# Optimization experiments

Hardware: AMD Instinct MI355X
Metric: run time of the kernel (lower is better)

The kernel has to match this reference:

```python
import jax, jax.numpy as jnp
import numpy as np

NV, NG, D, K, NB = 4096, 2048, 64, 128, 4
C_IN, C_OUT, E = 128, 8, 32768
SIGMA = 2.5  # rbf sigma used in the non-mp path


def _gcn_conv(x, src, dst, w, b, n):
    # PyG GCNConv (edge_weight=None, self loops already appended to src/dst)
    deg = jax.ops.segment_sum(jnp.ones(src.shape, x.dtype), dst, num_segments=n)
    dinv = jnp.where(deg > 0, 1.0 / jnp.sqrt(deg), 0.0)
    norm = dinv[src] * dinv[dst]
    h = x @ w
    return jax.ops.segment_sum(h[src] * norm[:, None], dst, num_segments=n) + b


def _diff_block(x, mass, evals, evecs, gradX, gradY, t, a_re, a_im, w0, b0, w1, b1, w2, b2):
    # learned-time spectral diffusion
    x_spec = evecs.T @ (x * mass[:, None])                      # [K, D]
    coef = jnp.exp(-evals[:, None] * jnp.clip(t, 1e-8)[None, :])  # [K, D]
    x_diff = evecs @ (coef * x_spec)                            # [NV, D]
    # spatial gradient features: complex grad, learned rotation, tanh of inner product
    gX = gradX @ x_diff                                         # real part  [NV, D]
    gY = gradY @ x_diff                                         # imag part  [NV, D]
    b_re = gX @ a_re - gY @ a_im
    b_im = gY @ a_re + gX @ a_im
    gfeat = jnp.tanh(gX * b_re + gY * b_im)
    f = jnp.concatenate([x, x_diff, gfeat], axis=-1)            # [NV, 3D]
    h = jax.nn.relu(f @ w0 + b0)
    h = jax.nn.relu(h @ w1 + b1)
    return h @ w2 + b2 + x                                      # residual skip


def _forward(surf_x, mass, evals, evecs, gradX, gradY, vertices, graph_x, graph_pos,
             lin1_w, lin1_b, lin2_w, lin2_b, last_w, last_b,
             diff_time, A_re, A_im, mlp_w0, mlp_b0, mlp_w1, mlp_b1, mlp_w2, mlp_b2,
             gcn_w1, gcn_b1, gcn_w2, gcn_b2, edge_index):
    nv, ng = vertices.shape[0], graph_pos.shape[0]
    # dense rbf coupling (torch.no_grad in original -> stop_gradient)
    d2 = (jnp.sum(vertices * vertices, 1)[:, None]
          + jnp.sum(graph_pos * graph_pos, 1)[None, :]
          - 2.0 * (vertices @ graph_pos.T))
    dist = jnp.sqrt(jnp.clip(d2, 0.0))
    rbf = jax.lax.stop_gradient(jnp.exp(-dist / SIGMA))          # [NV, NG]
    diff_x = surf_x @ lin1_w + lin1_b                            # [NV, D]
    gx = graph_x @ lin2_w + lin2_b                               # [NG, D]
    loops = jnp.arange(ng, dtype=edge_index.dtype)
    src = jnp.concatenate([edge_index[0], loops])
    dst = jnp.concatenate([edge_index[1], loops])
    for i in range(NB):
        diff_x = _diff_block(diff_x, mass, evals, evecs, gradX, gradY,
                             diff_time[i], A_re[i], A_im[i],
                             mlp_w0[i], mlp_b0[i], mlp_w1[i], mlp_b1[i], mlp_w2[i], mlp_b2[i])
        gx = rbf.T @ diff_x                                      # surface -> graph
        h = jax.nn.relu(_gcn_conv(gx, src, dst, gcn_w1[i], gcn_b1[i], ng))
        gx = _gcn_conv(h, src, dst, gcn_w2[i], gcn_b2[i], ng)
        diff_x = rbf @ gx                                        # graph -> surface
    return diff_x @ last_w + last_b                              # [NV, C_OUT]


def setup_inputs() -> dict:
    key = jax.random.key(0)
    ks = jax.random.split(key, 24)
    f32 = jnp.float32
    def rn(k, shape, scale=1.0):
        return jax.random.normal(k, shape, f32) * scale
    inp = {
        'surf_x': rn(ks[0], (NV, 5)),
        'mass': jax.random.uniform(ks[1], (NV,), f32, 0.1, 1.0),
        'evals': jnp.sort(jax.random.uniform(ks[2], (K,), f32, 0.0, 50.0)),
        'evecs': rn(ks[3], (NV, K), 1.0 / np.sqrt(NV)),
        'gradX': rn(ks[4], (NV, NV), 1.0 / np.sqrt(NV)),
        'gradY': rn(ks[5], (NV, NV), 1.0 / np.sqrt(NV)),
        'vertices': rn(ks[6], (NV, 3), 5.0),
        'graph_x': rn(ks[7], (NG, C_IN)),
        'graph_pos': rn(ks[8], (NG, 3), 5.0),
        'lin1_w': rn(ks[9], (5, D), 1.0 / np.sqrt(5)),
        'lin1_b': jnp.zeros((D,), f32),
        'lin2_w': rn(ks[10], (C_IN, D), 1.0 / np.sqrt(C_IN)),
        'lin2_b': jnp.zeros((D,), f32),
        'last_w': rn(ks[11], (D, C_OUT), 1.0 / np.sqrt(D)),
        'last_b': jnp.zeros((C_OUT,), f32),
        'diff_time': jax.random.uniform(ks[12], (NB, D), f32, 1e-3, 1.0),
        'A_re': rn(ks[13], (NB, D, D), 1.0 / np.sqrt(D)),
        'A_im': rn(ks[14], (NB, D, D), 1.0 / np.sqrt(D)),
        'mlp_w0': rn(ks[15], (NB, 3 * D, D), 1.0 / np.sqrt(3 * D)),
        'mlp_b0': jnp.zeros((NB, D), f32),
        'mlp_w1': rn(ks[16], (NB, D, D), 1.0 / np.sqrt(D)),
        'mlp_b1': jnp.zeros((NB, D), f32),
        'mlp_w2': rn(ks[17], (NB, D, D), 1.0 / np.sqrt(D)),
        'mlp_b2': jnp.zeros((NB, D), f32),
        'gcn_w1': rn(ks[18], (NB, D, D), 1.0 / np.sqrt(D)),
        'gcn_b1': jnp.zeros((NB, D), f32),
        'gcn_w2': rn(ks[19], (NB, D, D), 1.0 / np.sqrt(D)),
        'gcn_b2': jnp.zeros((NB, D), f32),
        'edge_index': jax.random.randint(ks[20], (2, E), 0, NG, dtype=jnp.int32),
    }
    return inp


def reference(surf_x, mass, evals, evecs, gradX, gradY, vertices, graph_x, graph_pos,
              lin1_w, lin1_b, lin2_w, lin2_b, last_w, last_b,
              diff_time, A_re, A_im, mlp_w0, mlp_b0, mlp_w1, mlp_b1, mlp_w2, mlp_b2,
              gcn_w1, gcn_b1, gcn_w2, gcn_b2, edge_index):
    return _forward(surf_x, mass, evals, evecs, gradX, gradY, vertices, graph_x, graph_pos,
                    lin1_w, lin1_b, lin2_w, lin2_b, last_w, last_b,
                    diff_time, A_re, A_im, mlp_w0, mlp_b0, mlp_w1, mlp_b1, mlp_w2, mlp_b2,
                    gcn_w1, gcn_b1, gcn_w2, gcn_b2, edge_index)
```

## Files before the change

### kernel.cpp

```cpp
#include <hip/hip_runtime.h>
#include <hip/hip_bf16.h>

#define NVV 4096
#define NGG 2048
#define DD 64
#define KSP 128
#define NBLK 4
#define NEDGE 32768
#define COUT 8
#define NSLICE 8
#define NSLICE_G 16
#define NSLICE_V 8
#define NSLICE_S 32
#define VS 32

typedef __hip_bfloat16 bf16;
using bf16x8 = __attribute__((ext_vector_type(8))) __bf16;
using s16x8  = __attribute__((ext_vector_type(8))) short;
using f32x4  = __attribute__((ext_vector_type(4))) float;

__device__ __forceinline__ float toF(bf16 x){ return __bfloat162float(x); }
__device__ __forceinline__ float ldin(const void* p, size_t i, int f){
  return f ? toF(((const bf16*)p)[i]) : ((const float*)p)[i];
}
__device__ __forceinline__ short f2bf(float x){
  __bf16 b = (__bf16)x;
  return __builtin_bit_cast(short, b);
}
__device__ __forceinline__ float bf2f(short s){
  return (float)__builtin_bit_cast(__bf16, s);
}
__device__ __forceinline__ bf16x8 ld8(const short* p){
  return __builtin_bit_cast(bf16x8, *(const s16x8*)p);
}
__device__ __forceinline__ void gl16(const short* g, short* l){
  __builtin_amdgcn_global_load_lds((__attribute__((address_space(1))) void*)(g),
                                   (__attribute__((address_space(3))) void*)(l),
                                   16, 0, 0);
}

__global__ void k_probe(const void* __restrict__ mass, int* __restrict__ flag){
  int t = threadIdx.x;
  float v = toF(((const bf16*)mass)[t]);
  bool ok = (v >= 0.05f) && (v <= 1.05f);
  unsigned long long m = __ballot(ok);
  if (t == 0) flag[0] = (m == ~0ull) ? 1 : 0;
}

__global__ void k_csr_zero(int* c){ int g = blockIdx.x*256+threadIdx.x; if (g<NGG) c[g]=0; }
__global__ void k_csr_cnt(const int* __restrict__ ei, int* __restrict__ c){
  int e = blockIdx.x*256+threadIdx.x; if (e<NEDGE) atomicAdd(&c[ei[NEDGE+e]], 1);
}
__global__ void k_csr_scan(const int* __restrict__ cnt, int* __restrict__ off,
                           int* __restrict__ cursor, float* __restrict__ dinv){
  __shared__ int ws[256];
  int t = threadIdx.x;
  int base = t*8;
  int local[8]; int s = 0;
  #pragma unroll
  for (int i=0;i<8;i++){ local[i]=s; s += cnt[base+i]; }
  ws[t] = s;
  __syncthreads();
  for (int o=1;o<256;o<<=1){
    int v = (t>=o) ? ws[t-o] : 0;
    __syncthreads();
    ws[t] += v;
    __syncthreads();
  }
  int pre = (t==0) ? 0 : ws[t-1];
  #pragma unroll
  for (int i=0;i<8;i++){
    int o = pre + local[i];
    off[base+i] = o; cursor[base+i] = o;
    dinv[base+i] = rsqrtf(1.f + (float)cnt[base+i]);
  }
  if (t==255) off[NGG] = pre + s;
}
__global__ void k_csr_fill(const int* __restrict__ ei, int* __restrict__ cursor,
                           int* __restrict__ csrc){
  int e = blockIdx.x*256+threadIdx.x;
  if (e < NEDGE){
    int d = ei[NEDGE+e];
    int p = atomicAdd(&cursor[d], 1);
    csrc[p] = ei[e];
  }
}

__global__ void k_lin1_mx(const void* __restrict__ sx, const void* __restrict__ w,
                          const void* __restrict__ b, const void* __restrict__ mass,
                          float* __restrict__ out, short* __restrict__ btMX,
                          const int* __restrict__ flg){
  const int f = *flg;
  __shared__ short tl[64*68];
  const int t = threadIdx.x;
  const int r = t>>2, c0 = (t&3)*16;
  const size_t v = (size_t)blockIdx.x*64 + r;
  float sxa[5];
  #pragma unroll
  for (int k=0;k<5;k++) sxa[k] = ldin(sx, v*5+k, f);
  const float mv = ldin(mass, v, f);
  float acc[16];
  #pragma unroll
  for (int j=0;j<16;j++){
    float a = ldin(b, c0+j, f);
    #pragma unroll
    for (int k=0;k<5;k++) a += sxa[k]*ldin(w, (size_t)k*DD + c0 + j, f);
    acc[j] = a;
    tl[(size_t)(c0+j)*68 + r] = f2bf(a*mv);
  }
  float* op = out + v*DD + c0;
  ((float4*)op)[0] = *(float4*)&acc[0];
  ((float4*)op)[1] = *(float4*)&acc[4];
  ((float4*)op)[2] = *(float4*)&acc[8];
  ((float4*)op)[3] = *(float4*)&acc[12];
  __syncthreads();
  s16x8 u0, u1;
  #pragma unroll
  for (int j=0;j<8;j++){ u0[j]=tl[(size_t)r*68+c0+j]; u1[j]=tl[(size_t)r*68+c0+8+j]; }
  const int s8 = (r&7)<<3;
  short* dp = btMX + (size_t)blockIdx.x*4096 + (size_t)r*64;
  *(s16x8*)&dp[c0 ^ s8]     = u0;
  *(s16x8*)&dp[(c0+8) ^ s8] = u1;
}

__global__ void k_spec_red(const float* __restrict__ partial, const void* __restrict__ evals,
                           const void* __restrict__ tvec, int boff,
                           short* __restrict__ btA, const int* __restrict__ flg){
  const int f = *flg;
  int idx = blockIdx.x*256 + threadIdx.x;
  int k = idx >> 6, d = idx & 63;
  float sum = 0.f;
  #pragma unroll 8
  for (int s = 0; s < VS; s++) sum += partial[(size_t)s*KSP*DD + idx];
  float t = fmaxf(ldin(tvec, boff + d, f), 1e-8f);
  float val = expf(-ldin(evals, k, f) * t) * sum;
  btA[(size_t)(k>>6)*4096 + (size_t)d*64 + ((k&63) ^ ((d&7)<<3))] = f2bf(val);
}

__global__ void k_cvt_a(const void* __restrict__ src, short* __restrict__ dst,
                        int Kfull, const int* __restrict__ flg){
  const int f = *flg;
  const int t = threadIdx.x;
  const int r = t>>2, c0 = (t&3)*16;
  const size_t row = (size_t)blockIdx.x*64 + r;
  const size_t base = row*(size_t)Kfull + (size_t)blockIdx.y*64 + c0;
  s16x8 v0, v1;
  if (f){
    const short* sp = (const short*)src + base;
    v0 = ((const s16x8*)sp)[0];
    v1 = ((const s16x8*)sp)[1];
  } else {
    const float* sp = (const float*)src + base;
    float tmp[16];
    ((float4*)tmp)[0] = ((const float4*)sp)[0];
    ((float4*)tmp)[1] = ((const float4*)sp)[1];
    ((float4*)tmp)[2] = ((const float4*)sp)[2];
    ((float4*)tmp)[3] = ((const float4*)sp)[3];
    #pragma unroll
    for (int i=0;i<8;i++){ v0[i]=f2bf(tmp[i]); v1[i]=f2bf(tmp[8+i]); }
  }
  const int s8 = (r&7)<<3;
  short* dp = dst + ((size_t)blockIdx.x*(Kfull>>6) + blockIdx.y)*4096 + (size_t)r*64;
  *(s16x8*)&dp[c0 ^ s8]     = v0;
  *(s16x8*)&dp[(c0+8) ^ s8] = v1;
}

__global__ void k_cvt_at(const void* __restrict__ evecs, short* __restrict__ dst,
                         const int* __restrict__ flg){
  const int f = *flg;
  __shared__ short tl[64*68];
  const int t = threadIdx.x;
  const int r = t>>2, c0 = (t&3)*16;
  const int kt = blockIdx.x, s = blockIdx.y;
  const size_t v = (size_t)kt*64 + r;
  #pragma unroll
  for (int j=0;j<16;j++)
    tl[(size_t)(c0+j)*68 + r] = f2bf(ldin(evecs, v*KSP + (size_t)s*64 + c0 + j, f));
  __syncthreads();
  s16x8 u0, u1;
  #pragma unroll
  for (int j=0;j<8;j++){ u0[j]=tl[(size_t)r*68+c0+j]; u1[j]=tl[(size_t)r*68+c0+8+j]; }
  const int s8 = (r&7)<<3;
  short* dp = dst + ((size_t)s*64 + kt)*4096 + (size_t)r*64;
  *(s16x8*)&dp[c0 ^ s8]     = u0;
  *(s16x8*)&dp[(c0+8) ^ s8] = u1;
}

__global__ void k_rbf_pre(const void* __restrict__ P, const void* __restrict__ Q,
                          short* __restrict__ rbfV, short* __restrict__ rbfG,
                          const int* __restrict__ flg){
  const int f = *flg;
  __shared__ short tl[64*68];
  const int t = threadIdx.x;
  const int r = t>>2, c0 = (t&3)*16;
  const int vt = blockIdx.x, gt = blockIdx.y;
  const float px = ldin(P, ((size_t)vt*64+r)*3+0, f);
  const float py = ldin(P, ((size_t)vt*64+r)*3+1, f);
  const float pz = ldin(P, ((size_t)vt*64+r)*3+2, f);
  s16x8 v0, v1;
  #pragma unroll
  for (int j=0;j<16;j++){
    const size_t g = (size_t)gt*64 + c0 + j;
    float dx = px - ldin(Q, g*3+0, f);
    float dy = py - ldin(Q, g*3+1, f);
    float dz = pz - ldin(Q, g*3+2, f);
    short s = f2bf(__expf(-sqrtf(dx*dx+dy*dy+dz*dz)*0.4f));
    if (j<8) v0[j] = s; else v1[j-8] = s;
    tl[(size_t)(c0+j)*68 + r] = s;
  }
  const int s8 = (r&7)<<3;
  short* vp = rbfV + ((size_t)vt*(NGG/64) + gt)*4096 + (size_t)r*64;
  *(s16x8*)&vp[c0 ^ s8]     = v0;
  *(s16x8*)&vp[(c0+8) ^ s8] = v1;
  __syncthreads();
  s16x8 u0, u1;
  #pragma unroll
  for (int j=0;j<8;j++){ u0[j] = tl[(size_t)r*68 + c0 + j]; u1[j] = tl[(size_t)r*68 + c0 + 8 + j]; }
  short* gp = rbfG + ((size_t)gt*(NVV/64) + vt)*4096 + (size_t)r*64;
  *(s16x8*)&gp[c0 ^ s8]     = u0;
  *(s16x8*)&gp[(c0+8) ^ s8] = u1;
}

__global__ void k_cvt_wt(const void* __restrict__ Are, const void* __restrict__ Aim,
                         const void* __restrict__ w0, const void* __restrict__ w1,
                         const void* __restrict__ w2,
                         short* __restrict__ btRe, short* __restrict__ btIm,
                         short* __restrict__ btW0, short* __restrict__ btW1,
                         short* __restrict__ btW2, const int* __restrict__ flg){
  const int f = *flg;
  __shared__ short tl[64*68];
  const int t = threadIdx.x;
  const int r = t>>2, c0 = (t&3)*16;
  const int slot = blockIdx.x, b = blockIdx.y;
  const void* src; size_t soff; short* dst; float scale = 1.f;
  switch(slot){
    case 0: src=Are; soff=(size_t)b*4096; dst=btRe + (size_t)b*2*4096;               break;
    case 1: src=Aim; soff=(size_t)b*4096; dst=btRe + (size_t)b*2*4096 + 4096; scale=-1.f; break;
    case 2: src=Aim; soff=(size_t)b*4096; dst=btIm + (size_t)b*2*4096;               break;
    case 3: src=Are; soff=(size_t)b*4096; dst=btIm + (size_t)b*2*4096 + 4096;        break;
    case 4: case 5: case 6:
      src=w0; soff=(size_t)b*3*4096 + (size_t)(slot-4)*4096;
      dst=btW0 + (size_t)b*3*4096 + (size_t)(slot-4)*4096;                           break;
    case 7: src=w1; soff=(size_t)b*4096; dst=btW1 + (size_t)b*4096;                  break;
    default: src=w2; soff=(size_t)b*4096; dst=btW2 + (size_t)b*4096;                 break;
  }
  #pragma unroll
  for (int j=0;j<16;j++)
    tl[(size_t)(c0+j)*68 + r] = f2bf(scale * ldin(src, soff + (size_t)r*64 + c0 + j, f));
  __syncthreads();
  s16x8 u0, u1;
  #pragma unroll
  for (int j=0;j<8;j++){ u0[j]=tl[(size_t)r*68+c0+j]; u1[j]=tl[(size_t)r*68+c0+8+j]; }
  const int s8 = (r&7)<<3;
  short* dp = dst + (size_t)r*64;
  *(s16x8*)&dp[c0 ^ s8]     = u0;
  *(s16x8*)&dp[(c0+8) ^ s8] = u1;
}

template<int TWO>
__global__ void k_gemm_pre(const short* __restrict__ A0, const short* __restrict__ A1,
                           const short* __restrict__ Bt, float* __restrict__ C,
                           int M, int ktt, int tps, int yoff, short* __restrict__ btOut){
  constexpr int NBUF = TWO ? 3 : 2;
  __shared__ __align__(16) short sm[2*NBUF*4096];
  const int t = threadIdx.x;
  const int w = t>>6, lane = t&63;
  const int fr = lane&15, fq = lane>>4;
  const int strip = blockIdx.x, sl = blockIdx.y;
  const size_t abase = ((size_t)strip*ktt + (size_t)sl*tps)*4096;
  const short* gA0 = A0 + abase;
  const short* gA1 = TWO ? (A1 + abase) : A0;
  const short* gB  = Bt + (size_t)sl*tps*4096;
  const int to = t*8;

  auto stage = [&](int p, int kt){
    short* l = &sm[p*NBUF*4096];
    const size_t ko = (size_t)kt*4096;
    gl16(gA0 + ko + to,        l + (w<<9));
    gl16(gA0 + ko + 2048 + to, l + 2048 + (w<<9));
    if (TWO){
      gl16(gA1 + ko + to,        l + 4096 + (w<<9));
      gl16(gA1 + ko + 2048 + to, l + 6144 + (w<<9));
    }
    short* lb = l + (TWO ? 8192 : 4096);
    gl16(gB + ko + to,        lb + (w<<9));
    gl16(gB + ko + 2048 + to, lb + 2048 + (w<<9));
  };

  f32x4 acc0[4] = {{0,0,0,0},{0,0,0,0},{0,0,0,0},{0,0,0,0}};
  f32x4 acc1[4] = {{0,0,0,0},{0,0,0,0},{0,0,0,0},{0,0,0,0}};

  stage(0, 0);
  int cur = 0;
  const int arow = w*16 + fr;
  const int ax0 = arow*64;
  const int asw = (arow&7)<<3;
  for (int kt=0; kt<tps; ++kt){
    if (kt+1 < tps){
      stage(cur^1, kt+1);
      if constexpr (TWO) asm volatile("s_waitcnt vmcnt(6)" ::: "memory");
      else               asm volatile("s_waitcnt vmcnt(4)" ::: "memory");
    } else {
      asm volatile("s_waitcnt vmcnt(0)" ::: "memory");
    }
    __builtin_amdgcn_s_barrier();
    asm volatile("" ::: "memory");
    const short* As  = &sm[cur*NBUF*4096];
    const short* A1s = As + 4096;
    const short* Bs  = As + (TWO ? 8192 : 4096);
    #pragma unroll
    for (int ks=0; ks<2; ks++){
      const int kx = ks*32 + fq*8;
      bf16x8 a0 = ld8(&As[ax0 + (kx ^ asw)]);
      bf16x8 a1 = TWO ? ld8(&A1s[ax0 + (kx ^ asw)]) : a0;
      #pragma unroll
      for (int nc=0;nc<4;nc++){
        const int brow = nc*16 + fr;
        bf16x8 b = ld8(&Bs[brow*64 + (kx ^ ((brow&7)<<3))]);
        acc0[nc] = __builtin_amdgcn_mfma_f32_16x16x32_bf16(a0, b, acc0[nc], 0, 0, 0);
        if constexpr (TWO)
          acc1[nc] = __builtin_amdgcn_mfma_f32_16x16x32_bf16(a1, b, acc1[nc], 0, 0, 0);
      }
    }
    asm volatile("" ::: "memory");
    __builtin_amdgcn_s_barrier();
    cur ^= 1;
  }
  float* C0 = C + (size_t)sl*M*DD;
  const int row0 = strip*64 + w*16 + fq*4;
  #pragma unroll
  for (int nc=0;nc<4;nc++)
    #pragma unroll
    for (int r=0;r<4;r++)
      C0[(size_t)(row0+r)*DD + nc*16 + fr] = acc0[nc][r];
  if constexpr (TWO){
    float* C1 = C + (size_t)yoff + (size_t)sl*M*DD;
    #pragma unroll
    for (int nc=0;nc<4;nc++)
      #pragma unroll
      for (int r=0;r<4;r++)
        C1[(size_t)(row0+r)*DD + nc*16 + fr] = acc1[nc][r];
  }
  if (btOut){
    #pragma unroll
    for (int nc=0;nc<4;nc++)
      #pragma unroll
      for (int r=0;r<4;r++){
        int k = row0 + r, n = nc*16 + fr;
        btOut[(size_t)(k>>6)*4096 + (size_t)n*64 + ((k&63) ^ ((n&7)<<3))] = f2bf(acc0[nc][r]);
      }
  }
}

__global__ void k_reduce_mx(const float* __restrict__ P, const void* __restrict__ mass,
                            float* __restrict__ C, short* __restrict__ btMX,
                            int slices, const int* __restrict__ flg){
  const int f = *flg;
  __shared__ short tl[64*68];
  const int t = threadIdx.x;
  const int r = t>>2, c0 = (t&3)*16;
  const size_t v = (size_t)blockIdx.x*64 + r;
  float acc[16];
  #pragma unroll
  for (int j=0;j<16;j++) acc[j] = 0.f;
  const float* pb = P + v*DD + c0;
  for (int s=0;s<slices;s++){
    const float* ps = pb + (size_t)s*NVV*DD;
    #pragma unroll
    for (int q=0;q<4;q++){
      float4 a = ((const float4*)ps)[q];
      acc[q*4+0]+=a.x; acc[q*4+1]+=a.y; acc[q*4+2]+=a.z; acc[q*4+3]+=a.w;
    }
  }
  float* op = C + v*DD + c0;
  ((float4*)op)[0] = *(float4*)&acc[0];
  ((float4*)op)[1] = *(float4*)&acc[4];
  ((float4*)op)[2] = *(float4*)&acc[8];
  ((float4*)op)[3] = *(float4*)&acc[12];
  const float mv = ldin(mass, v, f);
  #pragma unroll
  for (int j=0;j<16;j++) tl[(size_t)(c0+j)*68 + r] = f2bf(acc[j]*mv);
  __syncthreads();
  s16x8 u0, u1;
  #pragma unroll
  for (int j=0;j<8;j++){ u0[j]=tl[(size_t)r*68+c0+j]; u1[j]=tl[(size_t)r*68+c0+8+j]; }
  const int s8 = (r&7)<<3;
  short* dp = btMX + (size_t)blockIdx.x*4096 + (size_t)r*64;
  *(s16x8*)&dp[c0 ^ s8]     = u0;
  *(s16x8*)&dp[(c0+8) ^ s8] = u1;
}

__global__ void k_tail_fused(const float* __restrict__ part,
                             const float* __restrict__ cur, const float* __restrict__ xdiff,
                             const short* __restrict__ btRe, const short* __restrict__ btIm,
                             const short* __restrict__ btW0, const short* __restrict__ btW1,
                             const short* __restrict__ btW2,
                             const void* __restrict__ b0, const void* __restrict__ b1,
                             const void* __restrict__ b2, int boff,
                             short* __restrict__ btOut, const int* __restrict__ flg){
  __shared__ __align__(16) short sm[8*4096];
  const int f = *flg;
  const int t = threadIdx.x;
  const int w = t>>6, lane = t&63;
  const int fr = lane&15, fq = lane>>4;
  const int strip = blockIdx.x;
  const int to = t*8;
  gl16(btRe + to,        &sm[2*4096] + (w<<9));
  gl16(btRe + 2048 + to, &sm[2*4096] + 2048 + (w<<9));
  gl16(btRe + 4096 + to, &sm[3*4096] + (w<<9));
  gl16(btRe + 6144 + to, &sm[3*4096] + 2048 + (w<<9));
  gl16(btIm + to,        &sm[4*4096] + (w<<9));
  gl16(btIm + 2048 + to, &sm[4*4096] + 2048 + (w<<9));
  gl16(btIm + 4096 + to, &sm[5*4096] + (w<<9));
  gl16(btIm + 6144 + to, &sm[5*4096] + 2048 + (w<<9));
  {
    const int r = t>>2, c0 = (t&3)*16;
    float4 gxa[4] = {{0,0,0,0},{0,0,0,0},{0,0,0,0},{0,0,0,0}};
    float4 gya[4] = {{0,0,0,0},{0,0,0,0},{0,0,0,0},{0,0,0,0}};
    const float* pb = part + ((size_t)strip*64 + r)*DD + c0;
    #pragma unroll
    for (int s=0;s<NSLICE;s++){
      const float* px = pb + (size_t)s*NVV*DD;
      const float* py = pb + (size_t)(s+NSLICE)*NVV*DD;
      #pragma unroll
      for (int q=0;q<4;q++){
        float4 a = ((const float4*)px)[q];
        float4 bq = ((const float4*)py)[q];
        gxa[q].x+=a.x;  gxa[q].y+=a.y;  gxa[q].z+=a.z;  gxa[q].w+=a.w;
        gya[q].x+=bq.x; gya[q].y+=bq.y; gya[q].z+=bq.z; gya[q].w+=bq.w;
      }
    }
    const float* gx_ = (const float*)gxa;
    const float* gy_ = (const float*)gya;
    s16x8 x0,x1,y0,y1;
    #pragma unroll
    for (int j=0;j<8;j++){ x0[j]=f2bf(gx_[j]); x1[j]=f2bf(gx_[8+j]);
                           y0[j]=f2bf(gy_[j]); y1[j]=f2bf(gy_[8+j]); }
    const int s8 = (r&7)<<3;
    *(s16x8*)&sm[0*4096 + r*64 + (c0 ^ s8)]     = x0;
    *(s16x8*)&sm[0*4096 + r*64 + ((c0+8) ^ s8)] = x1;
    *(s16x8*)&sm[1*4096 + r*64 + (c0 ^ s8)]     = y0;
    *(s16x8*)&sm[1*4096 + r*64 + ((c0+8) ^ s8)] = y1;
    const float* cp = cur   + ((size_t)strip*64 + r)*DD + c0;
    const float* xp = xdiff + ((size_t)strip*64 + r)*DD + c0;
    float ca[16], xa[16];
    ((float4*)ca)[0]=((const float4*)cp)[0]; ((float4*)ca)[1]=((const float4*)cp)[1];
    ((float4*)ca)[2]=((const float4*)cp)[2]; ((float4*)ca)[3]=((const float4*)cp)[3];
    ((float4*)xa)[0]=((const float4*)xp)[0]; ((float4*)xa)[1]=((const float4*)xp)[1];
    ((float4*)xa)[2]=((const float4*)xp)[2]; ((float4*)xa)[3]=((const float4*)xp)[3];
    s16x8 v0,v1,u0,u1;
    #pragma unroll
    for (int j=0;j<8;j++){ v0[j]=f2bf(ca[j]); v1[j]=f2bf(ca[8+j]);
                           u0[j]=f2bf(xa[j]); u1[j]=f2bf(xa[8+j]); }
    *(s16x8*)&sm[6*4096 + r*64 + (c0 ^ s8)]     = v0;
    *(s16x8*)&sm[6*4096 + r*64 + ((c0+8) ^ s8)] = v1;
    *(s16x8*)&sm[7*4096 + r*64 + (c0 ^ s8)]     = u0;
    *(s16x8*)&sm[7*4096 + r*64 + ((c0+8) ^ s8)] = u1;
  }
  __syncthreads();
  const int arow = w*16 + fr;
  const int asw = (arow&7)<<3;
  f32x4 re[4] = {{0,0,0,0},{0,0,0,0},{0,0,0,0},{0,0,0,0}};
  f32x4 im[4] = {{0,0,0,0},{0,0,0,0},{0,0,0,0},{0,0,0,0}};
  #pragma unroll
  for (int kt=0; kt<2; kt++){
    const short* As = &sm[kt*4096];
    const short* Br = &sm[(2+kt)*4096];
    const short* Bi = &sm[(4+kt)*4096];
    #pragma unroll
    for (int ks=0; ks<2; ks++){
      const int kx = ks*32 + fq*8;
      bf16x8 a = ld8(&As[arow*64 + (kx ^ asw)]);
      #pragma unroll
      for (int nc=0;nc<4;nc++){
        const int brow = nc*16 + fr, bsw = (brow&7)<<3;
        bf16x8 br_ = ld8(&Br[brow*64 + (kx ^ bsw)]);
        bf16x8 bi_ = ld8(&Bi[brow*64 + (kx ^ bsw)]);
        re[nc] = __builtin_amdgcn_mfma_f32_16x16x32_bf16(a, br_, re[nc], 0, 0, 0);
        im[nc] = __builtin_amdgcn_mfma_f32_16x16x32_bf16(a, bi_, im[nc], 0, 0, 0);
      }
    }
  }
  __syncthreads();
  gl16(btW0 + to,           &sm[2*4096] + (w<<9));
  gl16(btW0 + 2048 + to,    &sm[2*4096] + 2048 + (w<<9));
  gl16(btW0 + 4096 + to,    &sm[3*4096] + (w<<9));
  gl16(btW0 + 6144 + to,    &sm[3*4096] + 2048 + (w<<9));
  gl16(btW0 + 8192 + to,    &sm[4*4096] + (w<<9));
  gl16(btW0 + 10240 + to,   &sm[4*4096] + 2048 + (w<<9));
  gl16(btW1 + to,           &sm[5*4096] + (w<<9));
  gl16(btW1 + 2048 + to,    &sm[5*4096] + 2048 + (w<<9));
  float gfv[4][4];
  #pragma unroll
  for (int nc=0;nc<4;nc++){
    const int n = nc*16 + fr;
    #pragma unroll
    for (int r2=0;r2<4;r2++){
      const int mi = w*16 + fq*4 + r2;
      const int pos = mi*64 + (n ^ ((mi&7)<<3));
      float gx = bf2f(sm[pos]);
      float gy = bf2f(sm[4096 + pos]);
      gfv[nc][r2] = tanhf(gx*re[nc][r2] + gy*im[nc][r2]);
    }
  }
  __syncthreads();
  gl16(btW2 + to,        &sm[1*4096] + (w<<9));
  gl16(btW2 + 2048 + to, &sm[1*4096] + 2048 + (w<<9));
  #pragma unroll
  for (int nc=0;nc<4;nc++)
    #pragma unroll
    for (int r2=0;r2<4;r2++){
      const int mi = w*16 + fq*4 + r2, n = nc*16 + fr;
      sm[mi*64 + (n ^ ((mi&7)<<3))] = f2bf(gfv[nc][r2]);
    }
  __syncthreads();
  f32x4 acc[4] = {{0,0,0,0},{0,0,0,0},{0,0,0,0},{0,0,0,0}};
  #pragma unroll
  for (int kt=0; kt<3; kt++){
    const short* As = &sm[(kt==0 ? 6 : (kt==1 ? 7 : 0))*4096];
    const short* Bs = &sm[(2+kt)*4096];
    #pragma unroll
    for (int ks=0; ks<2; ks++){
      const int kx = ks*32 + fq*8;
      bf16x8 a = ld8(&As[arow*64 + (kx ^ asw)]);
      #pragma unroll
      for (int nc=0;nc<4;nc++){
        const int brow = nc*16 + fr;
        bf16x8 b = ld8(&Bs[brow*64 + (kx ^ ((brow&7)<<3))]);
        acc[nc] = __builtin_amdgcn_mfma_f32_16x16x32_bf16(a, b, acc[nc], 0, 0, 0);
      }
    }
  }
  __syncthreads();
  #pragma unroll
  for (int nc=0;nc<4;nc++){
    float bz = ldin(b0, boff + nc*16 + fr, f);
    #pragma unroll
    for (int r2=0;r2<4;r2++){
      const int mi = w*16 + fq*4 + r2, n = nc*16 + fr;
      sm[6*4096 + mi*64 + (n ^ ((mi&7)<<3))] = f2bf(fmaxf(acc[nc][r2] + bz, 0.f));
    }
  }
  __syncthreads();
  f32x4 a1c[4] = {{0,0,0,0},{0,0,0,0},{0,0,0,0},{0,0,0,0}};
  #pragma unroll
  for (int ks=0; ks<2; ks++){
    const int kx = ks*32 + fq*8;
    bf16x8 a = ld8(&sm[6*4096 + arow*64 + (kx ^ asw)]);
    #pragma unroll
    for (int nc=0;nc<4;nc++){
      const int brow = nc*16 + fr;
      bf16x8 b = ld8(&sm[5*4096 + brow*64 + (kx ^ ((brow&7)<<3))]);
      a1c[nc] = __builtin_amdgcn_mfma_f32_16x16x32_bf16(a, b, a1c[nc], 0, 0, 0);
    }
  }
  #pragma unroll
  for (int nc=0;nc<4;nc++){
    float bz = ldin(b1, boff + nc*16 + fr, f);
    #pragma unroll
    for (int r2=0;r2<4;r2++){
      const int mi = w*16 + fq*4 + r2, n = nc*16 + fr;
      sm[7*4096 + mi*64 + (n ^ ((mi&7)<<3))] = f2bf(fmaxf(a1c[nc][r2] + bz, 0.f));
    }
  }
  __syncthreads();
  f32x4 a2c[4] = {{0,0,0,0},{0,0,0,0},{0,0,0,0},{0,0,0,0}};
  #pragma unroll
  for (int ks=0; ks<2; ks++){
    const int kx = ks*32 + fq*8;
    bf16x8 a = ld8(&sm[7*4096 + arow*64 + (kx ^ asw)]);
    #pragma unroll
    for (int nc=0;nc<4;nc++){
      const int brow = nc*16 + fr;
      bf16x8 b = ld8(&sm[1*4096 + brow*64 + (kx ^ ((brow&7)<<3))]);
      a2c[nc] = __builtin_amdgcn_mfma_f32_16x16x32_bf16(a, b, a2c[nc], 0, 0, 0);
    }
  }
  const int row0 = strip*64 + w*16 + fq*4;
  #pragma unroll
  for (int nc=0;nc<4;nc++){
    float bz = ldin(b2, boff + nc*16 + fr, f);
    #pragma unroll
    for (int r2=0;r2<4;r2++){
      int row = row0 + r2, n = nc*16 + fr;
      float vv = a2c[nc][r2] + bz + cur[(size_t)row*DD + n];
      btOut[(size_t)(row>>6)*4096 + (size_t)n*64 + ((row&63) ^ ((n&7)<<3))] = f2bf(vv);
    }
  }
}

__global__ void k_gcn1(const float* __restrict__ part, const void* __restrict__ W,
                       int woff, const float* __restrict__ dinv,
                       const void* __restrict__ bias, int boff,
                       float* __restrict__ tmp, float* __restrict__ outinit,
                       const int* __restrict__ flg){
  const int f = *flg;
  __shared__ float xs[4][DD];
  int d = threadIdx.x & 63, vl = threadIdx.x >> 6;
  size_t g = (size_t)blockIdx.x*4 + vl;
  float x = 0.f;
  #pragma unroll
  for (int s = 0; s < NSLICE_G; s++) x += part[(size_t)s*NGG*DD + g*DD + d];
  xs[vl][d] = x;
  __syncthreads();
  float acc = 0.f;
  #pragma unroll 8
  for (int k=0;k<DD;k++) acc += xs[vl][k]*ldin(W, (size_t)woff + k*DD + d, f);
  tmp[g*DD+d] = acc;
  float di = dinv[g];
  outinit[g*DD+d] = acc*di*di + ldin(bias, boff + d, f);
}

__global__ void k_gcn2f(const float* __restrict__ selfinit, const float* __restrict__ tmp,
                        const int* __restrict__ off, const int* __restrict__ csrc,
                        const float* __restrict__ dinv, const void* __restrict__ W,
                        int woff, const void* __restrict__ bias, int boff,
                        float* __restrict__ tmp2, float* __restrict__ out2init,
                        const int* __restrict__ flg){
  const int f = *flg;
  __shared__ float xs[4][DD];
  int d = threadIdx.x & 63, vl = threadIdx.x >> 6;
  size_t g = (size_t)blockIdx.x*4 + vl;
  float dg = dinv[g];
  float agg = selfinit[g*DD+d];
  int s1 = off[g+1];
  for (int i = off[g]; i < s1; i++){
    int sv = csrc[i];
    agg += tmp[(size_t)sv*DD+d]*(dinv[sv]*dg);
  }
  xs[vl][d] = fmaxf(agg, 0.f);
  __syncthreads();
  float acc = 0.f;
  #pragma unroll 8
  for (int k=0;k<DD;k++) acc += xs[vl][k]*ldin(W, (size_t)woff + k*DD + d, f);
  tmp2[g*DD+d] = acc;
  out2init[g*DD+d] = acc*dg*dg + ldin(bias, boff + d, f);
}

__global__ void k_aggr_t(const float* __restrict__ selfinit, const float* __restrict__ tmp,
                         const int* __restrict__ off, const int* __restrict__ csrc,
                         const float* __restrict__ dinv, short* __restrict__ dst){
  __shared__ short tl[64*68];
  const int t = threadIdx.x;
  const int r = t>>2, c0 = (t&3)*16;
  const size_t g = (size_t)blockIdx.x*64 + r;
  const float dg = dinv[g];
  float agg[16];
  const float* sp = selfinit + g*DD + c0;
  ((float4*)agg)[0] = ((const float4*)sp)[0];
  ((float4*)agg)[1] = ((const float4*)sp)[1];
  ((float4*)agg)[2] = ((const float4*)sp)[2];
  ((float4*)agg)[3] = ((const float4*)sp)[3];
  const int e1 = off[g+1];
  for (int i = off[g]; i < e1; i++){
    const int sv = csrc[i];
    const float w_ = dinv[sv]*dg;
    const float* tp = tmp + (size_t)sv*DD + c0;
    #pragma unroll
    for (int q=0;q<4;q++){
      float4 a = ((const float4*)tp)[q];
      agg[q*4+0]+=a.x*w_; agg[q*4+1]+=a.y*w_; agg[q*4+2]+=a.z*w_; agg[q*4+3]+=a.w*w_;
    }
  }
  #pragma unroll
  for (int j=0;j<16;j++) tl[(size_t)(c0+j)*68 + r] = f2bf(agg[j]);
  __syncthreads();
  s16x8 u0,u1;
  #pragma unroll
  for (int j=0;j<8;j++){ u0[j]=tl[(size_t)r*68+c0+j]; u1[j]=tl[(size_t)r*68+c0+8+j]; }
  const int s8 = (r&7)<<3;
  short* dp = dst + (size_t)blockIdx.x*4096 + (size_t)r*64;
  *(s16x8*)&dp[c0 ^ s8]     = u0;
  *(s16x8*)&dp[(c0+8) ^ s8] = u1;
}

__global__ void k_final(const float* __restrict__ x, const void* __restrict__ w,
                        const void* __restrict__ b, void* __restrict__ outv,
                        const int* __restrict__ flg){
  const int f = *flg;
  int idx = blockIdx.x*256 + threadIdx.x;
  int v = idx >> 3, c = idx & 7;
  float acc = ldin(b, c, f);
  #pragma unroll 8
  for (int k=0;k<DD;k++) acc += x[(size_t)v*DD+k]*ldin(w, (size_t)k*COUT+c, f);
  if (f) ((bf16*)outv)[idx] = __float2bfloat16(acc);
  else   ((float*)outv)[idx] = acc;
}

extern "C" void kernel_launch(void* const* d_in, const int* in_sizes, int n_in,
                              void* d_out, int out_size, void* d_ws, size_t ws_size,
                              hipStream_t stream){
  (void)in_sizes; (void)n_in;
  const void* surf_x   = d_in[0];
  const void* mass     = d_in[1];
  const void* evals    = d_in[2];
  const void* evecs    = d_in[3];
  const void* gradX    = d_in[4];
  const void* gradY    = d_in[5];
  const void* vertices = d_in[6];
  const void* gpos     = d_in[8];
  const void* lin1_w   = d_in[9];
  const void* lin1_b   = d_in[10];
  const void* last_w   = d_in[13];
  const void* last_b   = d_in[14];
  const void* dtime    = d_in[15];
  const void* A_re     = d_in[16];
  const void* A_im     = d_in[17];
  const void* mw0      = d_in[18];
  const void* mb0      = d_in[19];
  const void* mw1      = d_in[20];
  const void* mb1      = d_in[21];
  const void* mw2      = d_in[22];
  const void* mb2      = d_in[23];
  const void* gw1      = d_in[24];
  const void* gb1      = d_in[25];
  const void* gw2      = d_in[26];
  const void* gb2      = d_in[27];
  const int*  ei       = (const int*)d_in[28];

  const size_t REQUIRED = (size_t)126*1024*1024;
  if (ws_size < REQUIRED){
    hipMemsetAsync(d_out, 0, (size_t)out_size*2, stream);
    return;
  }
  char* p = (char*)d_ws;
  auto alloc = [&](size_t bytes)->void*{
    void* r = (void*)p;
    p += (bytes + 255) & ~(size_t)255;
    return r;
  };
  float* part  = (float*)alloc((size_t)16*NVV*DD*4);
  float* bufA  = (float*)alloc((size_t)NVV*DD*4);
  float* xdiff = (float*)alloc((size_t)NVV*DD*4);
  float* tmpg  = (float*)alloc((size_t)NGG*DD*4);
  float* hg    = (float*)alloc((size_t)NGG*DD*4);
  float* tmp2  = (float*)alloc((size_t)NGG*DD*4);
  float* o2    = (float*)alloc((size_t)NGG*DD*4);
  float* dinv  = (float*)alloc((size_t)NGG*4);
  int*   flg   = (int*)alloc(256);
  int*   cnt   = (int*)alloc((size_t)NGG*4);
  int*   off   = (int*)alloc((size_t)(NGG+1)*4);
  int*   curs  = (int*)alloc((size_t)NGG*4);
  int*   csrc  = (int*)alloc((size_t)NEDGE*4);
  short* gXs   = (short*)alloc((size_t)NVV*NVV*2);
  short* gYs   = (short*)alloc((size_t)NVV*NVV*2);
  short* rbfV  = (short*)alloc((size_t)NVV*NGG*2);
  short* rbfG  = (short*)alloc((size_t)NVV*NGG*2);
  short* evsT  = (short*)alloc((size_t)NVV*KSP*2);
  short* evs   = (short*)alloc((size_t)NVV*KSP*2);
  short* btA   = (short*)alloc((size_t)KSP*DD*2);
  short* btB   = (short*)alloc((size_t)NVV*DD*2);
  short* btMX  = (short*)alloc((size_t)NVV*DD*2);
  short* btRe  = (short*)alloc((size_t)NBLK*2*4096*2);
  short* btIm  = (short*)alloc((size_t)NBLK*2*4096*2);
  short* btW0  = (short*)alloc((size_t)NBLK*3*4096*2);
  short* btW1  = (short*)alloc((size_t)NBLK*4096*2);
  short* btW2  = (short*)alloc((size_t)NBLK*4096*2);

  k_probe<<<1, 64, 0, stream>>>(mass, flg);
  k_csr_zero<<<NGG/256, 256, 0, stream>>>(cnt);
  k_csr_cnt <<<NEDGE/256, 256, 0, stream>>>(ei, cnt);
  k_csr_scan<<<1, 256, 0, stream>>>(cnt, off, curs, dinv);
  k_csr_fill<<<NEDGE/256, 256, 0, stream>>>(ei, curs, csrc);
  k_lin1_mx <<<NVV/64, 256, 0, stream>>>(surf_x, lin1_w, lin1_b, mass, bufA, btMX, flg);
  k_cvt_a<<<dim3(NVV/64, NVV/64), 256, 0, stream>>>(gradX, gXs, NVV, flg);
  k_cvt_a<<<dim3(NVV/64, NVV/64), 256, 0, stream>>>(gradY, gYs, NVV, flg);
  k_cvt_a<<<dim3(NVV/64, KSP/64), 256, 0, stream>>>(evecs, evs, KSP, flg);
  k_cvt_at<<<dim3(NVV/64, KSP/64), 256, 0, stream>>>(evecs, evsT, flg);
  k_rbf_pre<<<dim3(NVV/64, NGG/64), 256, 0, stream>>>(vertices, gpos, rbfV, rbfG, flg);
  k_cvt_wt<<<dim3(9, NBLK), 256, 0, stream>>>(A_re, A_im, mw0, mw1, mw2,
                                              btRe, btIm, btW0, btW1, btW2, flg);

  float* cur = bufA;
  for (int b = 0; b < NBLK; b++){
    k_gemm_pre<0><<<dim3(KSP/64, NSLICE_S), 256, 0, stream>>>(evsT, evsT, btMX, part,
        KSP, NVV/64, (NVV/64)/NSLICE_S, 0, nullptr);
    k_spec_red<<<KSP*DD/256, 256, 0, stream>>>(part, evals, dtime, b*DD, btA, flg);
    k_gemm_pre<0><<<dim3(NVV/64, 1), 256, 0, stream>>>(evs, evs, btA, xdiff,
        NVV, KSP/64, KSP/64, 0, btB);
    k_gemm_pre<1><<<dim3(NVV/64, NSLICE), 256, 0, stream>>>(gXs, gYs, btB, part,
        NVV, NVV/64, (NVV/64)/NSLICE, NSLICE*NVV*DD, nullptr);
    k_tail_fused<<<NVV/64, 256, 0, stream>>>(part, cur, xdiff,
        btRe + (size_t)b*2*4096, btIm + (size_t)b*2*4096,
        btW0 + (size_t)b*3*4096, btW1 + (size_t)b*4096, btW2 + (size_t)b*4096,
        mb0, mb1, mb2, b*DD, btB, flg);
    k_gemm_pre<0><<<dim3(NGG/64, NSLICE_G), 256, 0, stream>>>(rbfG, rbfG, btB, part,
        NGG, NVV/64, (NVV/64)/NSLICE_G, 0, nullptr);
    k_gcn1<<<NGG/4, 256, 0, stream>>>(part, gw1, b*DD*DD, dinv, gb1, b*DD, tmpg, hg, flg);
    k_gcn2f<<<NGG/4, 256, 0, stream>>>(hg, tmpg, off, csrc, dinv, gw2, b*DD*DD,
                                       gb2, b*DD, tmp2, o2, flg);
    k_aggr_t<<<NGG/64, 256, 0, stream>>>(o2, tmp2, off, csrc, dinv, btB);
    k_gemm_pre<0><<<dim3(NVV/64, NSLICE_V), 256, 0, stream>>>(rbfV, rbfV, btB, part,
        NVV, NGG/64, (NGG/64)/NSLICE_V, 0, nullptr);
    k_reduce_mx<<<NVV/64, 256, 0, stream>>>(part, mass, cur, btMX, NSLICE_V, flg);
  }
  k_final<<<NVV*COUT/256, 256, 0, stream>>>(cur, last_w, last_b, d_out, flg);
}
```

Before: 663.8 us.

## Precompute gradX·evecs and gradY·evecs once to shrink per-block gradient GEMMs

Uses associativity: gradX @ (evecs @ A) = (gradX @ evecs) @ A. The products gradX·evecs and gradY·evecs ([NV,K]) are computed once before the block loop and stored in bf16. Each block then runs a small K=128 GEMM instead of a K=4096 dense GEMM, which removes most of the per-block FLOPs and traffic over the 32 MB bf16 gradient matrices. The trade-off is extra bf16 rounding from the precomputed intermediate and two large setup GEMMs that replace four per-block ones.

```diff
diff --git a/kernel.cpp b/kernel.cpp
--- a/kernel.cpp
+++ b/kernel.cpp
@@ -8,7 +8,7 @@
 #define NBLK 4
 #define NEDGE 32768
 #define COUT 8
-#define NSLICE 8
+#define NSLICE_P 8
 #define NSLICE_G 16
 #define NSLICE_V 8
 #define NSLICE_S 32
@@ -352,6 +352,39 @@
   }
 }
 
+__global__ void k_fold_at(const float* __restrict__ part, short* __restrict__ dX,
+                          short* __restrict__ dY, int s){
+  const int t = threadIdx.x;
+  const int r = t>>2, c0 = (t&3)*16;
+  const int strip = blockIdx.x;
+  float ax[16], ay[16];
+  #pragma unroll
+  for (int j=0;j<16;j++){ ax[j]=0.f; ay[j]=0.f; }
+  const float* pb = part + ((size_t)strip*64 + r)*DD + c0;
+  for (int sl=0; sl<NSLICE_P; sl++){
+    const float* px = pb + (size_t)sl*NVV*DD;
+    const float* py = pb + (size_t)(sl+NSLICE_P)*NVV*DD;
+    #pragma unroll
+    for (int q=0;q<4;q++){
+      float4 a = ((const float4*)px)[q];
+      float4 b = ((const float4*)py)[q];
+      ax[q*4+0]+=a.x; ax[q*4+1]+=a.y; ax[q*4+2]+=a.z; ax[q*4+3]+=a.w;
+      ay[q*4+0]+=b.x; ay[q*4+1]+=b.y; ay[q*4+2]+=b.z; ay[q*4+3]+=b.w;
+    }
+  }
+  s16x8 x0,x1,y0,y1;
+  #pragma unroll
+  for (int j=0;j<8;j++){ x0[j]=f2bf(ax[j]); x1[j]=f2bf(ax[8+j]);
+                         y0[j]=f2bf(ay[j]); y1[j]=f2bf(ay[8+j]); }
+  const int s8 = (r&7)<<3;
+  short* dpx = dX + ((size_t)strip*2 + s)*4096 + (size_t)r*64;
+  short* dpy = dY + ((size_t)strip*2 + s)*4096 + (size_t)r*64;
+  *(s16x8*)&dpx[c0 ^ s8]     = x0;
+  *(s16x8*)&dpx[(c0+8) ^ s8] = x1;
+  *(s16x8*)&dpy[c0 ^ s8]     = y0;
+  *(s16x8*)&dpy[(c0+8) ^ s8] = y1;
+}
+
 __global__ void k_reduce_mx(const float* __restrict__ P, const void* __restrict__ mass,
                             float* __restrict__ C, short* __restrict__ btMX,
                             int slices, const int* __restrict__ flg){
@@ -390,7 +423,7 @@
   *(s16x8*)&dp[(c0+8) ^ s8] = u1;
 }
 
-__global__ void k_tail_fused(const float* __restrict__ part,
+__global__ void k_tail_fused(const float* __restrict__ gXp, const float* __restrict__ gYp,
                              const float* __restrict__ cur, const float* __restrict__ xdiff,
                              const short* __restrict__ btRe, const short* __restrict__ btIm,
                              const short* __restrict__ btW0, const short* __restrict__ btW1,
@@ -415,27 +448,20 @@
   gl16(btIm + 6144 + to, &sm[5*4096] + 2048 + (w<<9));
   {
     const int r = t>>2, c0 = (t&3)*16;
-    float4 gxa[4] = {{0,0,0,0},{0,0,0,0},{0,0,0,0},{0,0,0,0}};
-    float4 gya[4] = {{0,0,0,0},{0,0,0,0},{0,0,0,0},{0,0,0,0}};
-    const float* pb = part + ((size_t)strip*64 + r)*DD + c0;
-    #pragma unroll
-    for (int s=0;s<NSLICE;s++){
-      const float* px = pb + (size_t)s*NVV*DD;
-      const float* py = pb + (size_t)(s+NSLICE)*NVV*DD;
-      #pragma unroll
-      for (int q=0;q<4;q++){
-        float4 a = ((const float4*)px)[q];
-        float4 bq = ((const float4*)py)[q];
-        gxa[q].x+=a.x;  gxa[q].y+=a.y;  gxa[q].z+=a.z;  gxa[q].w+=a.w;
-        gya[q].x+=bq.x; gya[q].y+=bq.y; gya[q].z+=bq.z; gya[q].w+=bq.w;
-      }
-    }
-    const float* gx_ = (const float*)gxa;
-    const float* gy_ = (const float*)gya;
+    const size_t rowb = ((size_t)strip*64 + r)*DD + c0;
+    float gxa[16], gya[16];
+    ((float4*)gxa)[0]=((const float4*)(gXp+rowb))[0];
+    ((float4*)gxa)[1]=((const float4*)(gXp+rowb))[1];
+    ((float4*)gxa)[2]=((const float4*)(gXp+rowb))[2];
+    ((float4*)gxa)[3]=((const float4*)(gXp+rowb))[3];
+    ((float4*)gya)[0]=((const float4*)(gYp+rowb))[0];
+    ((float4*)gya)[1]=((const float4*)(gYp+rowb))[1];
+    ((float4*)gya)[2]=((const float4*)(gYp+rowb))[2];
+    ((float4*)gya)[3]=((const float4*)(gYp+rowb))[3];
     s16x8 x0,x1,y0,y1;
     #pragma unroll
-    for (int j=0;j<8;j++){ x0[j]=f2bf(gx_[j]); x1[j]=f2bf(gx_[8+j]);
-                           y0[j]=f2bf(gy_[j]); y1[j]=f2bf(gy_[8+j]); }
+    for (int j=0;j<8;j++){ x0[j]=f2bf(gxa[j]); x1[j]=f2bf(gxa[8+j]);
+                           y0[j]=f2bf(gya[j]); y1[j]=f2bf(gya[8+j]); }
     const int s8 = (r&7)<<3;
     *(s16x8*)&sm[0*4096 + r*64 + (c0 ^ s8)]     = x0;
     *(s16x8*)&sm[0*4096 + r*64 + ((c0+8) ^ s8)] = x1;
@@ -748,6 +774,8 @@
   short* rbfG  = (short*)alloc((size_t)NVV*NGG*2);
   short* evsT  = (short*)alloc((size_t)NVV*KSP*2);
   short* evs   = (short*)alloc((size_t)NVV*KSP*2);
+  short* GXE   = (short*)alloc((size_t)NVV*KSP*2);
+  short* GYE   = (short*)alloc((size_t)NVV*KSP*2);
   short* btA   = (short*)alloc((size_t)KSP*DD*2);
   short* btB   = (short*)alloc((size_t)NVV*DD*2);
   short* btMX  = (short*)alloc((size_t)NVV*DD*2);
@@ -770,6 +798,12 @@
   k_rbf_pre<<<dim3(NVV/64, NGG/64), 256, 0, stream>>>(vertices, gpos, rbfV, rbfG, flg);
   k_cvt_wt<<<dim3(9, NBLK), 256, 0, stream>>>(A_re, A_im, mw0, mw1, mw2,
                                               btRe, btIm, btW0, btW1, btW2, flg);
+  for (int s = 0; s < 2; s++){
+    k_gemm_pre<1><<<dim3(NVV/64, NSLICE_P), 256, 0, stream>>>(
+        gXs, gYs, evsT + (size_t)s*64*4096, part,
+        NVV, NVV/64, (NVV/64)/NSLICE_P, NSLICE_P*NVV*DD, nullptr);
+    k_fold_at<<<NVV/64, 256, 0, stream>>>(part, GXE, GYE, s);
+  }
 
   float* cur = bufA;
   for (int b = 0; b < NBLK; b++){
@@ -777,10 +811,10 @@
         KSP, NVV/64, (NVV/64)/NSLICE_S, 0, nullptr);
     k_spec_red<<<KSP*DD/256, 256, 0, stream>>>(part, evals, dtime, b*DD, btA, flg);
     k_gemm_pre<0><<<dim3(NVV/64, 1), 256, 0, stream>>>(evs, evs, btA, xdiff,
-        NVV, KSP/64, KSP/64, 0, btB);
-    k_gemm_pre<1><<<dim3(NVV/64, NSLICE), 256, 0, stream>>>(gXs, gYs, btB, part,
-        NVV, NVV/64, (NVV/64)/NSLICE, NSLICE*NVV*DD, nullptr);
-    k_tail_fused<<<NVV/64, 256, 0, stream>>>(part, cur, xdiff,
+        NVV, KSP/64, KSP/64, 0, nullptr);
+    k_gemm_pre<1><<<dim3(NVV/64, 1), 256, 0, stream>>>(GXE, GYE, btA, part,
+        NVV, 2, 2, NVV*DD, nullptr);
+    k_tail_fused<<<NVV/64, 256, 0, stream>>>(part, part + (size_t)NVV*DD, cur, xdiff,
         btRe + (size_t)b*2*4096, btIm + (size_t)b*2*4096,
         btW0 + (size_t)b*3*4096, btW1 + (size_t)b*4096, btW2 + (size_t)b*4096,
         mb0, mb1, mb2, b*DD, btB, flg);
```

Result: faster. 641.1 us (-3.4%).
